# Kernel optimization log

Hardware: AMD Instinct MI355X
Metric: run time of the kernel (lower is better)

## Reference

```python
import jax, jax.numpy as jnp
import numpy as np

LMAX = 2
NC = (LMAX + 1) ** 2          # 9 spherical-harmonic coefficients
C = 128                       # sphere/hidden channels (scalar_dim = 256//2)
CIN = 256                     # input/output irrep channels
EC = 16                       # edge channels (attn_weight_input_dim//2)
N_ATOM = 512
TOPK = 8
E = N_ATOM * TOPK
RES = 18                      # SO3 grid resolution

# m-primary permutation from CoefficientMapping(lmax=2, mmax=2).to_m:
# m=0 real [0,2,6]; m=1 real [3,7]; m=1 imag [1,5]; m=2 real [8]; m=2 imag [4]
PERM = np.array([0, 2, 6, 3, 7, 1, 5, 8, 4])
INV_PERM = np.argsort(PERM)
DEG = np.array([0, 1, 1, 1, 2, 2, 2, 2, 2])  # degree l of each coefficient


def _so2_block(em, x_edge, d0w, d0b, m0w1, m0w2,
               m1dw, m1db, m1w1r, m1w2r, m1w1i, m1w2i,
               m2dw, m2db, m2w1r, m2w2r, m2w1i, m2w2i):
    # em: [E, 9, C] (l-primary); x_edge: [E, EC]
    En = em.shape[0]
    em = em[:, PERM]                                  # -> m-primary order
    # m = 0 block (3 coefficients)
    g0 = jax.nn.silu(x_edge @ d0w + d0b)              # [E, C]
    x0 = em[:, 0:3].reshape(En, 3 * C)
    x0 = (((x0 @ m0w1) * g0) @ m0w2).reshape(En, 3, C)

    def so2_conv(xm, dw, db, w1r, w2r, w1i, w2i):
        # xm: [E, 2, k*C] with (real, imag) stacked on axis 1
        ge = jax.nn.silu(x_edge @ dw + db).reshape(En, 2, C)
        xr = jnp.einsum('eti,ih->eth', xm, w1r) * ge[:, 0:1]
        xr = jnp.einsum('eth,ho->eto', xr, w2r)
        xi = jnp.einsum('eti,ih->eth', xm, w1i) * ge[:, 1:2]
        xi = jnp.einsum('eth,ho->eto', xi, w2i)
        return jnp.stack([xr[:, 0] - xi[:, 1], xr[:, 1] + xi[:, 0]], axis=1)

    x1 = so2_conv(em[:, 3:7].reshape(En, 2, 2 * C), m1dw, m1db, m1w1r, m1w2r, m1w1i, m1w2i).reshape(En, 4, C)
    x2 = so2_conv(em[:, 7:9].reshape(En, 2, C), m2dw, m2db, m2w1r, m2w2r, m2w1i, m2w2i).reshape(En, 2, C)
    em = jnp.concatenate([x0, x1, x2], axis=1)
    return em[:, INV_PERM]                            # back to l-primary


def _forward(x, attn_weight, wigner, to_grid, from_grid, w_in, b_in, w_out, b_out,
             emb_src, emb_tgt, fc_dist_w, fc_dist_b, fc_edge_w, fc_edge_b,
             so2_dist0_w, so2_dist0_b, so2_m0_w1, so2_m0_w2,
             so2_m1_dist_w, so2_m1_dist_b, so2_m1_w1r, so2_m1_w2r, so2_m1_w1i, so2_m1_w2i,
             so2_m2_dist_w, so2_m2_dist_b, so2_m2_w1r, so2_m2_w2r, so2_m2_w1i, so2_m2_w2i,
             atomic_numbers, edge_src, attn_mask):
    N, topK = attn_weight.shape[:2]
    Eg = N * topK
    # proj_input: per-degree SO3 linear 256 -> 128, bias on l=0 only
    h = jnp.einsum('nic,ico->nio', x, w_in[DEG])
    h = h.at[:, 0, :].add(b_in)
    edge_tgt = jnp.repeat(jnp.arange(N), topK)
    # edge feature: dist MLP + source/target atom-type embedding gathers
    xe = attn_weight.reshape(Eg, -1) @ fc_dist_w + fc_dist_b
    xe = xe + emb_src[atomic_numbers][edge_src] + emb_tgt[atomic_numbers][edge_tgt]
    xe = jax.nn.silu(jax.nn.silu(xe) @ fc_edge_w + fc_edge_b)
    # gather node features to edges + rotate into edge frame (Wigner D)
    xs = jnp.einsum('eij,ejc->eic', wigner, h[edge_src])
    xt = jnp.einsum('eij,ejc->eic', wigner, h[edge_tgt])

    def blk(b, em):
        return _so2_block(em, xe, so2_dist0_w[b], so2_dist0_b[b], so2_m0_w1[b], so2_m0_w2[b],
                          so2_m1_dist_w[b], so2_m1_dist_b[b], so2_m1_w1r[b], so2_m1_w2r[b], so2_m1_w1i[b], so2_m1_w2i[b],
                          so2_m2_dist_w[b], so2_m2_dist_b[b], so2_m2_w1r[b], so2_m2_w2r[b], so2_m2_w1i[b], so2_m2_w2i[b])

    xt = blk(0, xs) + blk(1, xt)
    # grid activation: to-grid, SiLU, from-grid
    xg = jax.nn.silu(jnp.einsum('bai,eic->ebac', to_grid, xt))
    xt = jnp.einsum('bai,ebac->eic', from_grid, xg)
    # inverse rotation (orthogonal Wigner -> transpose)
    xt = jnp.einsum('eji,ejc->eic', wigner, xt)
    # mask invalid neighbors, scatter-sum over topK
    out = xt.reshape(N, topK, NC, C)
    out = jnp.where(attn_mask[:, :, None, None], 0.0, out).sum(axis=1)
    # proj_final: per-degree SO3 linear 128 -> 256
    out = jnp.einsum('nic,ico->nio', out, w_out[DEG])
    return out.at[:, 0, :].add(b_out)


def setup_inputs() -> dict:
    key = jax.random.key(0)
    ks = jax.random.split(key, 40)
    s = 0.05
    inp = {
        'x': jax.random.normal(ks[0], (N_ATOM, NC, CIN), jnp.float32),
        'attn_weight': jax.random.normal(ks[1], (N_ATOM, TOPK, 32), jnp.float32),
        'wigner': jax.random.normal(ks[2], (E, NC, NC), jnp.float32) * 0.3,
        'to_grid': jax.random.normal(ks[3], (RES, RES, NC), jnp.float32) * 0.2,
        'from_grid': jax.random.normal(ks[4], (RES, RES, NC), jnp.float32) * 0.2,
        'w_in': jax.random.normal(ks[5], (3, CIN, C), jnp.float32) * s,
        'b_in': jax.random.normal(ks[6], (C,), jnp.float32) * s,
        'w_out': jax.random.normal(ks[7], (3, C, CIN), jnp.float32) * s,
        'b_out': jax.random.normal(ks[8], (CIN,), jnp.float32) * s,
        'emb_src': jax.random.uniform(ks[9], (256, EC), jnp.float32, -0.001, 0.001),
        'emb_tgt': jax.random.uniform(ks[10], (256, EC), jnp.float32, -0.001, 0.001),
        'fc_dist_w': jax.random.normal(ks[11], (32, EC), jnp.float32) * s,
        'fc_dist_b': jax.random.normal(ks[12], (EC,), jnp.float32) * s,
        'fc_edge_w': jax.random.normal(ks[13], (EC, EC), jnp.float32) * s,
        'fc_edge_b': jax.random.normal(ks[14], (EC,), jnp.float32) * s,
        'so2_dist0_w': jax.random.normal(ks[15], (2, EC, C), jnp.float32) * s,
        'so2_dist0_b': jax.random.normal(ks[16], (2, C), jnp.float32) * s,
        'so2_m0_w1': jax.random.normal(ks[17], (2, 3 * C, C), jnp.float32) * s,
        'so2_m0_w2': jax.random.normal(ks[18], (2, C, 3 * C), jnp.float32) * s,
        'so2_m1_dist_w': jax.random.normal(ks[19], (2, EC, 2 * C), jnp.float32) * s,
        'so2_m1_dist_b': jax.random.normal(ks[20], (2, 2 * C), jnp.float32) * s,
        'so2_m1_w1r': jax.random.normal(ks[21], (2, 2 * C, C), jnp.float32) * s,
        'so2_m1_w2r': jax.random.normal(ks[22], (2, C, 2 * C), jnp.float32) * s,
        'so2_m1_w1i': jax.random.normal(ks[23], (2, 2 * C, C), jnp.float32) * s,
        'so2_m1_w2i': jax.random.normal(ks[24], (2, C, 2 * C), jnp.float32) * s,
        'so2_m2_dist_w': jax.random.normal(ks[25], (2, EC, 2 * C), jnp.float32) * s,
        'so2_m2_dist_b': jax.random.normal(ks[26], (2, 2 * C), jnp.float32) * s,
        'so2_m2_w1r': jax.random.normal(ks[27], (2, C, C), jnp.float32) * s,
        'so2_m2_w2r': jax.random.normal(ks[28], (2, C, C), jnp.float32) * s,
        'so2_m2_w1i': jax.random.normal(ks[29], (2, C, C), jnp.float32) * s,
        'so2_m2_w2i': jax.random.normal(ks[30], (2, C, C), jnp.float32) * s,
        'atomic_numbers': jax.random.randint(ks[31], (N_ATOM,), 0, 256),
        'edge_src': jax.random.randint(ks[32], (E,), 0, N_ATOM),
        'attn_mask': jax.random.randint(ks[33], (N_ATOM, TOPK), 0, 2).astype(bool),
    }
    return inp


def reference(x, attn_weight, wigner, to_grid, from_grid, w_in, b_in, w_out, b_out,
              emb_src, emb_tgt, fc_dist_w, fc_dist_b, fc_edge_w, fc_edge_b,
              so2_dist0_w, so2_dist0_b, so2_m0_w1, so2_m0_w2,
              so2_m1_dist_w, so2_m1_dist_b, so2_m1_w1r, so2_m1_w2r, so2_m1_w1i, so2_m1_w2i,
              so2_m2_dist_w, so2_m2_dist_b, so2_m2_w1r, so2_m2_w2r, so2_m2_w1i, so2_m2_w2i,
              atomic_numbers, edge_src, attn_mask):
    return _forward(x, attn_weight, wigner, to_grid, from_grid, w_in, b_in, w_out, b_out,
                    emb_src, emb_tgt, fc_dist_w, fc_dist_b, fc_edge_w, fc_edge_b,
                    so2_dist0_w, so2_dist0_b, so2_m0_w1, so2_m0_w2,
                    so2_m1_dist_w, so2_m1_dist_b, so2_m1_w1r, so2_m1_w2r, so2_m1_w1i, so2_m1_w2i,
                    so2_m2_dist_w, so2_m2_dist_b, so2_m2_w1r, so2_m2_w2r, so2_m2_w1i, so2_m2_w2i,
                    atomic_numbers, edge_src, attn_mask)
```

## Files before the change

### kernel.cpp

```cpp
#include <hip/hip_runtime.h>
#include <math.h>

typedef __attribute__((ext_vector_type(8))) short short8;
typedef __attribute__((ext_vector_type(4))) short short4_t;
typedef __attribute__((ext_vector_type(4))) float f32x4;

__device__ const int d_PERM[9] = {0,2,6,3,7,1,5,8,4};
__device__ const int d_DEG[9]  = {0,1,1,1,2,2,2,2,2};

__device__ __forceinline__ float silu_f(float x){ return x / (1.0f + __expf(-x)); }

__device__ __forceinline__ unsigned short f2bf(float f){
  unsigned int u = __float_as_uint(f);
  return (unsigned short)((u + 0x7FFFu + ((u >> 16) & 1u)) >> 16);
}

__device__ __forceinline__ int mask_at(const void* mp, int flag, int e){
  if (flag==1) return ((const unsigned char*)mp)[e] != 0;
  if (flag==3) return ((const unsigned int*)mp)[2*e] != 0u;
  return ((const unsigned int*)mp)[e] != 0u;
}

__global__ void k_detect(const unsigned int* __restrict__ w, int* __restrict__ flag){
  __shared__ int notI, notF, anyOdd, anyEven;
  if (threadIdx.x==0){ notI=0; notF=0; anyOdd=0; anyEven=0; }
  __syncthreads();
  int li=0, lf=0, lo=0, le=0;
  for (int i = threadIdx.x; i < 1024; i += 256){
    unsigned int v = w[i];
    if (v != 0u && v != 1u) li = 1;
    if (v != 0u && v != 0x3F800000u) lf = 1;
    if (v != 0u){ if (i & 1) lo = 1; else le = 1; }
  }
  if (li) atomicOr(&notI,1);
  if (lf) atomicOr(&notF,1);
  if (lo) atomicOr(&anyOdd,1);
  if (le) atomicOr(&anyEven,1);
  __syncthreads();
  if (threadIdx.x==0){
    int f;
    if (!notI) f = (anyOdd || !anyEven) ? 0 : 3;
    else       f = (!notF) ? 2 : 1;
    *flag = f;
  }
}

__global__ __launch_bounds__(256) void k_compact(const void* __restrict__ maskp,
    const int* __restrict__ flagp, int* __restrict__ list, int* __restrict__ count){
  __shared__ int cnt[256];
  __shared__ int offs[256];
  int f = *flagp;
  int tid = threadIdx.x;
  int base = tid*16;
  int c = 0;
  for (int i=0;i<16;i++) if (!mask_at(maskp, f, base+i)) c++;
  cnt[tid] = c;
  __syncthreads();
  if (tid==0){
    int r = 0;
    for (int i=0;i<256;i++){ offs[i] = r; r += cnt[i]; }
    *count = r;
  }
  __syncthreads();
  int w = offs[tid];
  for (int i=0;i<16;i++){
    int e = base+i;
    if (!mask_at(maskp, f, e)) list[w++] = e;
  }
}

__global__ __launch_bounds__(128) void k_h(const float* __restrict__ x,
    const float* __restrict__ w_in, const float* __restrict__ b_in,
    float* __restrict__ H){
  __shared__ float xl[16][260];
  int i = blockIdx.y; int n0 = blockIdx.x*16;
  int deg = d_DEG[i];
  for (int idx = threadIdx.x; idx < 16*256; idx += 128){
    int r = idx >> 8, c = idx & 255;
    xl[r][c] = x[((size_t)(n0+r)*9 + i)*256 + c];
  }
  __syncthreads();
  int o = threadIdx.x;
  float acc[16];
  #pragma unroll
  for (int r=0;r<16;r++) acc[r]=0.f;
  const float* w = w_in + (size_t)deg*32768 + o;
  for (int c=0;c<256;c+=4){
    float w0=w[(size_t)c*128], w1=w[(size_t)(c+1)*128], w2=w[(size_t)(c+2)*128], w3=w[(size_t)(c+3)*128];
    #pragma unroll
    for (int r=0;r<16;r++){
      float4 xv4 = *(const float4*)&xl[r][c];
      acc[r] += xv4.x*w0 + xv4.y*w1 + xv4.z*w2 + xv4.w*w3;
    }
  }
  float bb = (i==0)? b_in[o] : 0.f;
  #pragma unroll
  for (int r=0;r<16;r++) H[((size_t)(n0+r)*9+i)*128+o] = acc[r]+bb;
}

__global__ __launch_bounds__(256) void k_xe(const float* __restrict__ attn,
    const float* __restrict__ fdw, const float* __restrict__ fdb,
    const float* __restrict__ few, const float* __restrict__ feb,
    const float* __restrict__ es, const float* __restrict__ et,
    const int* __restrict__ an, const int* __restrict__ esrc,
    float* __restrict__ XE){
  int e = blockIdx.x*256 + threadIdx.x;
  float aw[32];
  #pragma unroll
  for (int k=0;k<32;k+=4){
    float4 v = *(const float4*)&attn[(size_t)e*32+k];
    aw[k]=v.x; aw[k+1]=v.y; aw[k+2]=v.z; aw[k+3]=v.w;
  }
  int src = esrc[e]; int tgt = e>>3;
  int za = an[src], zb = an[tgt];
  float v0[16];
  #pragma unroll
  for (int j=0;j<16;j++){
    float s = fdb[j] + es[(size_t)za*16+j] + et[(size_t)zb*16+j];
    #pragma unroll
    for (int k=0;k<32;k++) s += aw[k]*fdw[k*16+j];
    v0[j] = silu_f(s);
  }
  #pragma unroll
  for (int j=0;j<16;j++){
    float s = feb[j];
    #pragma unroll
    for (int k=0;k<16;k++) s += v0[k]*few[k*16+j];
    XE[(size_t)e*16+j] = silu_f(s);
  }
}

__global__ __launch_bounds__(256) void k_wcvt(
    const float* __restrict__ m0w1, const float* __restrict__ m1w1r, const float* __restrict__ m1w1i,
    const float* __restrict__ m2w1r, const float* __restrict__ m2w1i,
    const float* __restrict__ m0w2, const float* __restrict__ m1w2r, const float* __restrict__ m1w2i,
    const float* __restrict__ m2w2r, const float* __restrict__ m2w2i,
    unsigned short* __restrict__ Wt)
{
  int base = (blockIdx.x*256 + threadIdx.x)*4;
  #pragma unroll
  for (int ii = 0; ii < 4; ii++){
    int idx = base + ii;
    float v;
    if (idx < 98304){
      int p = idx/49152, r = idx%49152, n = r/384, k = r%384;
      v = m0w1[p*49152 + k*128 + n];
    } else if (idx < 229376){
      int j = idx-98304; int q = j/32768, r = j%32768, n = r/256, k = r%256;
      const float* w = (q&1)?m1w1i:m1w1r;
      v = w[(q>>1)*32768 + k*128 + n];
    } else if (idx < 294912){
      int j = idx-229376; int q = j/16384, r = j%16384, n = r/128, k = r%128;
      const float* w = (q&1)?m2w1i:m2w1r;
      v = w[(q>>1)*16384 + k*128 + n];
    } else if (idx < 393216){
      int j = idx-294912; int n = j/256, k = j%256;
      v = m0w2[(k>>7)*49152 + (k&127)*384 + n];
    } else if (idx < 524288){
      int j = idx-393216; int n = j/512, k = j%512;
      const float* w = ((k>>7)&1)?m1w2i:m1w2r;
      v = w[(k>>8)*32768 + (k&127)*256 + n];
    } else {
      int j = idx-524288; int n = j/512, k = j%512;
      const float* w = ((k>>7)&1)?m2w2i:m2w2r;
      v = w[(k>>8)*16384 + (k&127)*128 + n];
    }
    Wt[idx] = f2bf(v);
  }
}

__global__ __launch_bounds__(256) void k_fprep(const float* __restrict__ tg,
    const float* __restrict__ fg,
    unsigned short* __restrict__ tgA, unsigned short* __restrict__ fgA)
{
  for (int idx = threadIdx.x; idx < 11264; idx += 256){
    int pt = idx >> 9, rem = idx & 511, l = rem >> 3, j = rem & 7;
    int p = pt*16 + (l & 15);
    int i = (l >> 4)*8 + j;
    float v = (p < 324 && i < 9) ? tg[p*9 + i] : 0.f;
    tgA[idx] = f2bf(v);
  }
  for (int idx = threadIdx.x; idx < 5632; idx += 256){
    int sb = idx >> 9, rem = idx & 511, l = rem >> 3, j = rem & 7;
    int p = sb*32 + (l >> 4)*8 + j;
    int i = l & 15;
    float v = (p < 324 && i < 9) ? fg[p*9 + i] : 0.f;
    fgA[idx] = f2bf(v);
  }
}

__global__ __launch_bounds__(256) void k_rotgate_m(
    const float* __restrict__ Hg, const float* __restrict__ XEg,
    const int* __restrict__ esrc, const float* __restrict__ wig,
    const float* __restrict__ d0w,  const float* __restrict__ d0b,
    const float* __restrict__ m1dw, const float* __restrict__ m1db,
    const float* __restrict__ m2dw, const float* __restrict__ m2db,
    unsigned short* __restrict__ XSb, unsigned short* __restrict__ XTb,
    float* __restrict__ G,
    const int* __restrict__ list, const int* __restrict__ countp, int s0)
{
  int slot = s0 + blockIdx.x;
  if (slot >= *countp) return;
  __shared__ float xe16[16];
  int e = list[slot];
  int el = blockIdx.x;
  int tid = threadIdx.x;
  int n = e >> 3, src = esrc[e];
  if (tid < 16) xe16[tid] = XEg[(size_t)e*16 + tid];
  for (int idx = tid; idx < 1152; idx += 256){
    int p = idx >> 7, c = idx & 127;
    int ch = d_PERM[p];
    const float* wr = wig + (size_t)e*81 + ch*9;
    const float* hs = Hg + (size_t)src*1152 + c;
    const float* ht = Hg + (size_t)n*1152 + c;
    float s1 = 0.f, s2 = 0.f;
    #pragma unroll
    for (int j = 0; j < 9; j++){
      float wv = wr[j];
      s1 += wv * hs[j*128];
      s2 += wv * ht[j*128];
    }
    XSb[(size_t)el*1152 + idx] = f2bf(s1);
    XTb[(size_t)el*1152 + idx] = f2bf(s2);
  }
  __syncthreads();
  for (int col = tid; col < 1280; col += 256){
    int b = col / 640, r = col % 640;
    const float* w; float bias; int ldw, c2;
    if (r < 128){       w = d0w  + (size_t)b*2048; c2 = r;     ldw = 128; bias = d0b[b*128 + c2]; }
    else if (r < 384){  w = m1dw + (size_t)b*4096; c2 = r-128; ldw = 256; bias = m1db[b*256 + c2]; }
    else {              w = m2dw + (size_t)b*4096; c2 = r-384; ldw = 256; bias = m2db[b*256 + c2]; }
    float s = bias;
    #pragma unroll
    for (int kk = 0; kk < 16; kk++) s += xe16[kk] * w[kk*ldw + c2];
    G[(size_t)el*1280 + col] = silu_f(s);
  }
}

__global__ __launch_bounds__(256) void k_gs1m(
    const unsigned short* __restrict__ XSb, const unsigned short* __restrict__ XTb,
    const float* __restrict__ G, const unsigned short* __restrict__ Wt,
    unsigned short* __restrict__ Pgb,
    const int* __restrict__ countp, int s0)
{
  int lc = *countp - s0;
  if (lc <= 0) return;
  if (lc > 2048) lc = 2048;
  int b = blockIdx.x, t = threadIdx.x;
  const unsigned short* Ax; const unsigned short* Bw;
  int K, bm, obase, goff, rsh, aoff, tstride;
  if (b < 64){
    int path = b & 1, mt = b >> 1;
    Ax = path ? XTb : XSb;
    Bw = Wt + path*49152;
    K = 384; bm = mt*64; obase = path*128; goff = path ? 640 : 0;
    rsh = 0; aoff = 0; tstride = 0;
  } else if (b < 320){
    int i = b-64; int q = i>>6, mt = i&63;
    Ax = (q>=2) ? XTb : XSb;
    Bw = Wt + 98304 + q*32768;
    K = 256; bm = mt*64; obase = 256 + q*256; goff = 128 + (q&1)*128 + (q>>1)*640;
    rsh = 1; aoff = 384; tstride = 256;
  } else {
    int i = b-320; int q = i>>6, mt = i&63;
    Ax = (q>=2) ? XTb : XSb;
    Bw = Wt + 229376 + q*16384;
    K = 128; bm = mt*64; obase = 1280 + q*256; goff = 384 + (q&1)*128 + (q>>1)*640;
    rsh = 1; aoff = 896; tstride = 128;
  }
  int rows = rsh ? 2*lc : lc;
  if (bm >= rows) return;
  int w = t >> 6, l = t & 63;
  int am = bm + w*16 + (l & 15);
  int ael = am >> rsh, atp = am & rsh;
  const unsigned short* aptr = Ax + (size_t)ael*1152 + aoff + atp*tstride + ((l>>4)*8);
  int bn = l & 15;
  int bko = (l>>4)*8;
  f32x4 acc[8];
  #pragma unroll
  for (int i=0;i<8;i++){ acc[i][0]=0.f; acc[i][1]=0.f; acc[i][2]=0.f; acc[i][3]=0.f; }
  for (int k0 = 0; k0 < K; k0 += 32){
    short8 a = *(const short8*)(aptr + k0);
    #pragma unroll
    for (int nt = 0; nt < 8; nt++){
      const unsigned short* bp = Bw + (size_t)(nt*16 + bn)*K + k0 + bko;
      short8 bb = *(const short8*)bp;
      acc[nt] = __builtin_amdgcn_mfma_f32_16x16x32_bf16(a, bb, acc[nt], 0, 0, 0);
    }
  }
  #pragma unroll
  for (int nt = 0; nt < 8; nt++){
    #pragma unroll
    for (int r = 0; r < 4; r++){
      int i2 = (l>>4)*4 + r;
      int m = bm + w*16 + i2;
      int el = m >> rsh, tp = m & rsh;
      int h = nt*16 + (l & 15);
      float v = acc[nt][r] * G[(size_t)el*1280 + goff + h];
      Pgb[(size_t)el*2304 + obase + tp*128 + h] = f2bf(v);
    }
  }
}

__global__ __launch_bounds__(256) void k_gs2m(
    const unsigned short* __restrict__ Pgb, const unsigned short* __restrict__ Wt2,
    unsigned short* __restrict__ Ybt,
    const int* __restrict__ countp, int s0)
{
  int lc = *countp - s0;
  if (lc <= 0) return;
  if (lc > 2048) lc = 2048;
  int b = blockIdx.x, t = threadIdx.x;
  int region, bm, ncb, K, rsh, segb;
  const unsigned short* Bw;
  if (b < 96){ region=0; int mt=b/3, nt3=b-mt*3; bm=mt*64; ncb=nt3*128; K=256; rsh=0; segb=0;    Bw = Wt2; }
  else if (b < 224){ region=1; int i=b-96; int mt=i>>1, nt2=i&1; bm=mt*64; ncb=nt2*128; K=512; rsh=1; segb=256;  Bw = Wt2 + 98304; }
  else { region=2; int mt=b-224; bm=mt*64; ncb=0; K=512; rsh=1; segb=1280; Bw = Wt2 + 229376; }
  int rows = rsh ? 2*lc : lc;
  if (bm >= rows) return;
  int w = t >> 6, l = t & 63;
  int am = bm + w*16 + (l & 15);
  int ael = am >> rsh, atp = am & rsh;
  int bko = (l>>4)*8;
  f32x4 acc[8];
  #pragma unroll
  for (int i=0;i<8;i++){ acc[i][0]=0.f; acc[i][1]=0.f; acc[i][2]=0.f; acc[i][3]=0.f; }
  for (int k0 = 0; k0 < K; k0 += 32){
    const unsigned short* ap;
    short sm = 0;
    if (region == 0){
      ap = Pgb + (size_t)ael*2304 + k0 + bko;
    } else {
      int seg = k0 >> 7, kk = k0 & 127;
      int tsel = (seg&1) ? (1-atp) : atp;
      sm = (short)(((seg&1) && atp==0) ? 0x8000 : 0);
      ap = Pgb + (size_t)ael*2304 + segb + seg*256 + tsel*128 + kk + bko;
    }
    short8 a = *(const short8*)ap;
    short8 smv = (short8)sm;
    a ^= smv;
    #pragma unroll
    for (int nt = 0; nt < 8; nt++){
      const unsigned short* bp = Bw + (size_t)(ncb + nt*16 + (l&15))*K + k0 + bko;
      short8 bb = *(const short8*)bp;
      acc[nt] = __builtin_amdgcn_mfma_f32_16x16x32_bf16(a, bb, acc[nt], 0, 0, 0);
    }
  }
  #pragma unroll
  for (int nt = 0; nt < 8; nt++){
    #pragma unroll
    for (int r = 0; r < 4; r++){
      int i2 = (l>>4)*4 + r;
      int m = bm + w*16 + i2;
      int el = m >> rsh, tp = m & rsh;
      int col = ncb + nt*16 + (l&15);
      int g = col >> 7, c = col & 127;
      int ch;
      if (region==0)      ch = (g==0) ? 0 : ((g==1) ? 2 : 6);
      else if (region==1) ch = tp ? (g ? 5 : 1) : (g ? 7 : 3);
      else                ch = tp ? 4 : 8;
      Ybt[(size_t)(s0 + el)*2048 + c*16 + ch] = f2bf(acc[nt][r]);
    }
  }
}

__global__ __launch_bounds__(256) void k_gridm(
    const unsigned short* __restrict__ Ybt,
    const unsigned short* __restrict__ tgA, const unsigned short* __restrict__ fgA,
    const float* __restrict__ wig,
    const int* __restrict__ list, const int* __restrict__ countp,
    float* __restrict__ R)
{
  int slot = blockIdx.x;
  if (slot >= *countp) return;
  __shared__ float wl[81];
  __shared__ unsigned short Sld[4][512];
  __shared__ float Zld[4][256];
  int tid = threadIdx.x;
  int e = list[slot];
  for (int i = tid; i < 81; i += 256) wl[i] = wig[(size_t)e*81 + i];
  __syncthreads();
  int w = tid >> 6, l = tid & 63;
  int lcn = l & 15, lg = l >> 4;
  const unsigned short* ybase = Ybt + (size_t)slot*2048;

  for (int ct = 0; ct < 2; ct++){
    int c0 = (w*2 + ct)*16;
    short8 bfA = (short8)(short)0;
    if (lg < 2) bfA = *(const short8*)(ybase + (c0 + lcn)*16 + lg*8);
    f32x4 Z; Z[0]=0.f; Z[1]=0.f; Z[2]=0.f; Z[3]=0.f;
    for (int sb = 0; sb < 11; sb++){
      f32x4 s0; s0[0]=0.f; s0[1]=0.f; s0[2]=0.f; s0[3]=0.f;
      f32x4 s1 = s0;
      short8 a0 = *(const short8*)(tgA + (size_t)(sb*2+0)*512 + l*8);
      short8 a1 = *(const short8*)(tgA + (size_t)(sb*2+1)*512 + l*8);
      s0 = __builtin_amdgcn_mfma_f32_16x16x32_bf16(a0, bfA, s0, 0, 0, 0);
      s1 = __builtin_amdgcn_mfma_f32_16x16x32_bf16(a1, bfA, s1, 0, 0, 0);
      short4_t pk0, pk1;
      #pragma unroll
      for (int r = 0; r < 4; r++){
        float v0 = s0[r]; v0 = v0 * __fdividef(1.0f, 1.0f + __expf(-v0));
        float v1 = s1[r]; v1 = v1 * __fdividef(1.0f, 1.0f + __expf(-v1));
        pk0[r] = (short)f2bf(v0);
        pk1[r] = (short)f2bf(v1);
      }
      *(short4_t*)&Sld[w][lcn*32 + lg*4]      = pk0;
      *(short4_t*)&Sld[w][lcn*32 + 16 + lg*4] = pk1;
      short8 af = *(const short8*)(fgA + (size_t)sb*512 + l*8);
      short8 bs = *(const short8*)&Sld[w][lcn*32 + lg*8];
      Z = __builtin_amdgcn_mfma_f32_16x16x32_bf16(af, bs, Z, 0, 0, 0);
    }
    *(f32x4*)&Zld[w][lcn*16 + lg*4] = Z;
    float zc[9];
    #pragma unroll
    for (int j = 0; j < 9; j++) zc[j] = Zld[w][lcn*16 + j];
    #pragma unroll
    for (int t2 = 0; t2 < 3; t2++){
      int i2 = lg + t2*4;
      if (i2 < 9){
        float r = 0.f;
        #pragma unroll
        for (int j = 0; j < 9; j++) r += wl[j*9 + i2] * zc[j];
        R[(size_t)e*1152 + i2*128 + c0 + lcn] = r;
      }
    }
  }
}

__global__ __launch_bounds__(256) void k_redout2(const float* __restrict__ R,
    const void* __restrict__ maskp, const int* __restrict__ flagp,
    const float* __restrict__ w_out, const float* __restrict__ b_out,
    float* __restrict__ out){
  __shared__ float sacc[128];
  int i2 = blockIdx.x; int n = blockIdx.y;
  int tid = threadIdx.x;
  int f = *flagp;
  if (tid < 128){
    float a = 0.f;
    for (int k = 0; k < 8; k++){
      int e = n*8 + k;
      if (!mask_at(maskp, f, e)) a += R[(size_t)e*1152 + i2*128 + tid];
    }
    sacc[tid] = a;
  }
  __syncthreads();
  int o = tid;
  int deg = d_DEG[i2];
  const float* wp = w_out + (size_t)deg*32768 + o;
  float s = (i2==0) ? b_out[o] : 0.f;
  #pragma unroll 4
  for (int c = 0; c < 128; c += 4){
    float4 a = *(const float4*)&sacc[c];
    s += a.x*wp[(size_t)c*256] + a.y*wp[(size_t)(c+1)*256]
       + a.z*wp[(size_t)(c+2)*256] + a.w*wp[(size_t)(c+3)*256];
  }
  out[((size_t)n*9 + i2)*256 + o] = s;
}

__device__ __forceinline__ float dotW(const float* __restrict__ A, const float* __restrict__ Wm, int K){
  float s = 0.f;
  #pragma unroll 4
  for (int i=0;i<K;i+=4){
    float4 a = *(const float4*)&A[i];
    s += a.x*Wm[(size_t)i*128] + a.y*Wm[(size_t)(i+1)*128]
       + a.z*Wm[(size_t)(i+2)*128] + a.w*Wm[(size_t)(i+3)*128];
  }
  return s;
}
__device__ __forceinline__ float dot2W(const float* __restrict__ P0, const float* __restrict__ P1,
    const float* __restrict__ W0, const float* __restrict__ W1, int ldw){
  float s = 0.f;
  #pragma unroll 4
  for (int k=0;k<128;k+=4){
    float4 a = *(const float4*)&P0[k];
    float4 b = *(const float4*)&P1[k];
    s += a.x*W0[(size_t)k*ldw] + a.y*W0[(size_t)(k+1)*ldw] + a.z*W0[(size_t)(k+2)*ldw] + a.w*W0[(size_t)(k+3)*ldw];
    s += b.x*W1[(size_t)k*ldw] + b.y*W1[(size_t)(k+1)*ldw] + b.z*W1[(size_t)(k+2)*ldw] + b.w*W1[(size_t)(k+3)*ldw];
  }
  return s;
}

__global__ __launch_bounds__(256) void k_mega(
    const float* __restrict__ x,      const float* __restrict__ w_in,  const float* __restrict__ b_in,
    const float* __restrict__ attn,
    const float* __restrict__ fdw,    const float* __restrict__ fdb,
    const float* __restrict__ few,    const float* __restrict__ feb,
    const float* __restrict__ es,     const float* __restrict__ et,
    const int*   __restrict__ an,     const int*   __restrict__ esrc,
    const float* __restrict__ d0w,    const float* __restrict__ d0b,
    const float* __restrict__ m1dw,   const float* __restrict__ m1db,
    const float* __restrict__ m2dw,   const float* __restrict__ m2db,
    const float* __restrict__ m0w1,   const float* __restrict__ m0w2,
    const float* __restrict__ m1w1r,  const float* __restrict__ m1w2r,
    const float* __restrict__ m1w1i,  const float* __restrict__ m1w2i,
    const float* __restrict__ m2w1r,  const float* __restrict__ m2w2r,
    const float* __restrict__ m2w1i,  const float* __restrict__ m2w2i,
    const float* __restrict__ wig,    const float* __restrict__ tg,   const float* __restrict__ fg,
    const float* __restrict__ w_out,  const float* __restrict__ b_out,
    const void*  __restrict__ maskp,  const int* __restrict__ flagp,
    float* __restrict__ out)
{
  __shared__ float S[7168];
  float* acc  = S;
  float* xs   = S + 1152;
  float* xtl  = S + 2304;
  float* Zb   = S + 1152;
  float* gg   = S + 3456;
  float* Yb   = S + 3456;
  float* P    = S + 4736;
  float* wl   = S + 7040;
  float* xe16 = S + 7124;
  float* xv   = S + 7140;

  const int n   = blockIdx.x;
  const int tid = threadIdx.x;
  const int f   = *flagp;

  for (int i = tid; i < 1152; i += 256) acc[i] = 0.f;

  for (int k = 0; k < 8; k++){
    int e = n*8 + k;
    if (mask_at(maskp, f, e)) continue;
    int src = esrc[e];
    __syncthreads();
    for (int i = tid; i < 81; i += 256) wl[i] = wig[(size_t)e*81 + i];
    if (tid < 16){
      int j = tid;
      float s = fdb[j] + es[(size_t)an[src]*16 + j] + et[(size_t)an[n]*16 + j];
      for (int kk = 0; kk < 32; kk++) s += attn[(size_t)e*32 + kk] * fdw[kk*16 + j];
      xv[j] = silu_f(s);
    }
    for (int idx = tid; idx < 2304; idx += 256){
      int which = idx >= 1152;
      int lidx = idx - which*1152;
      int j = lidx >> 7, c = lidx & 127;
      int deg = d_DEG[j];
      const float* wp = w_in + (size_t)deg*32768 + c;
      const float* xp = x + ((size_t)(which ? n : src)*9 + j)*256;
      float s = (j==0) ? b_in[c] : 0.f;
      for (int cc = 0; cc < 256; cc++) s += xp[cc] * wp[cc*128];
      P[idx] = s;
    }
    __syncthreads();
    if (tid < 16){
      int j = tid;
      float s = feb[j];
      for (int kk = 0; kk < 16; kk++) s += xv[kk] * few[kk*16 + j];
      xe16[j] = silu_f(s);
    }
    for (int idx = tid; idx < 1152; idx += 256){
      int p = idx >> 7, c = idx & 127;
      int ch = d_PERM[p];
      float s1 = 0.f, s2 = 0.f;
      #pragma unroll
      for (int j = 0; j < 9; j++){
        float wv = wl[ch*9 + j];
        s1 += wv * P[j*128 + c];
        s2 += wv * P[1152 + j*128 + c];
      }
      xs[idx]  = s1;
      xtl[idx] = s2;
    }
    __syncthreads();
    for (int col = tid; col < 1280; col += 256){
      int b = col / 640, r = col % 640;
      const float* w; float bias; int ldw, c2;
      if (r < 128){       w = d0w  + (size_t)b*2048; c2 = r;     ldw = 128; bias = d0b[b*128 + c2]; }
      else if (r < 384){  w = m1dw + (size_t)b*4096; c2 = r-128; ldw = 256; bias = m1db[b*256 + c2]; }
      else {              w = m2dw + (size_t)b*4096; c2 = r-384; ldw = 256; bias = m2db[b*256 + c2]; }
      float s = bias;
      #pragma unroll
      for (int kk = 0; kk < 16; kk++) s += xe16[kk] * w[kk*ldw + c2];
      gg[col] = silu_f(s);
    }
    __syncthreads();
    for (int o = tid; o < 2304; o += 256){
      float s;
      if (o < 256){
        int path = o >> 7, h = o & 127;
        s = dotW(path ? xtl : xs, m0w1 + (size_t)path*49152 + h, 384);
      } else if (o < 1280){
        int q = (o-256) >> 8; int rem = (o-256) & 255; int t = rem >> 7, h = rem & 127;
        const float* A  = ((q>=2) ? xtl : xs) + 384 + t*256;
        const float* Wm = ((q&1) ? m1w1i : m1w1r) + (size_t)((q>=2)?1:0)*32768 + h;
        s = dotW(A, Wm, 256);
      } else {
        int q = (o-1280) >> 8; int rem = (o-1280) & 255; int t = rem >> 7, h = rem & 127;
        const float* A  = ((q>=2) ? xtl : xs) + 896 + t*128;
        const float* Wm = ((q&1) ? m2w1i : m2w1r) + (size_t)((q>=2)?1:0)*16384 + h;
        s = dotW(A, Wm, 128);
      }
      P[o] = s;
    }
    __syncthreads();
    for (int o = tid; o < 2304; o += 256){
      int h = o & 127, goff;
      if (o < 256) goff = (o >> 7) ? 640 : 0;
      else if (o < 1280){ int q = (o-256) >> 8;  goff = 128 + (q&1)*128 + (q>>1)*640; }
      else              { int q = (o-1280) >> 8; goff = 384 + (q&1)*128 + (q>>1)*640; }
      P[o] *= gg[goff + h];
    }
    __syncthreads();
    for (int o = tid; o < 1152; o += 256){
      float s; int ch, c;
      if (o < 384){
        int g = o >> 7; c = o & 127;
        ch = (g==0) ? 0 : ((g==1) ? 2 : 6);
        const float* w0 = m0w2 + o;
        s = dot2W(P, P+128, w0, w0+49152, 384);
      } else if (o < 896){
        int om = o - 384; int tp = om >> 8; int col = om & 255;
        int g = col >> 7; c = col & 127;
        ch = tp ? (g ? 5 : 1) : (g ? 7 : 3);
        float sgn = tp ? 1.f : -1.f;
        const float* wr = m1w2r + col;
        const float* wi = m1w2i + col;
        s = dot2W(P+256+tp*128,     P+768+tp*128,     wr, wr+32768, 256)
          + sgn * dot2W(P+512+(1-tp)*128, P+1024+(1-tp)*128, wi, wi+32768, 256);
      } else {
        int om = o - 896; int tp = om >> 7; c = om & 127;
        ch = tp ? 4 : 8;
        float sgn = tp ? 1.f : -1.f;
        const float* wr = m2w2r + c;
        const float* wi = m2w2i + c;
        s = dot2W(P+1280+tp*128,     P+1792+tp*128,     wr, wr+16384, 128)
          + sgn * dot2W(P+1536+(1-tp)*128, P+2048+(1-tp)*128, wi, wi+16384, 128);
      }
      Yb[ch*128 + c] = s;
    }
    __syncthreads();
    {
      int half = tid >> 7, c = tid & 127;
      float z[9];
      #pragma unroll
      for (int i = 0; i < 9; i++) z[i] = 0.f;
      float y[9];
      #pragma unroll
      for (int i = 0; i < 9; i++) y[i] = Yb[i*128 + c];
      int p0 = half*162, p1 = p0 + 162;
      #pragma unroll 2
      for (int p = p0; p < p1; p++){
        float gp = 0.f;
        #pragma unroll
        for (int i = 0; i < 9; i++) gp += tg[p*9 + i] * y[i];
        float s = silu_f(gp);
        #pragma unroll
        for (int i = 0; i < 9; i++) z[i] += fg[p*9 + i] * s;
      }
      #pragma unroll
      for (int i = 0; i < 9; i++) Zb[half*1152 + i*128 + c] = z[i];
    }
    __syncthreads();
    for (int idx = tid; idx < 1152; idx += 256){
      int i2 = idx >> 7, c = idx & 127;
      float s = 0.f;
      #pragma unroll
      for (int j = 0; j < 9; j++)
        s += wl[j*9 + i2] * (Zb[j*128 + c] + Zb[1152 + j*128 + c]);
      acc[idx] += s;
    }
  }
  __syncthreads();
  {
    int o = tid;
    for (int i2 = 0; i2 < 9; i2++){
      int deg = d_DEG[i2];
      const float* wp = w_out + (size_t)deg*32768 + o;
      float s = (i2==0) ? b_out[o] : 0.f;
      #pragma unroll 4
      for (int c = 0; c < 128; c += 4){
        float4 a = *(const float4*)&acc[i2*128 + c];
        s += a.x*wp[(size_t)c*256] + a.y*wp[(size_t)(c+1)*256]
           + a.z*wp[(size_t)(c+2)*256] + a.w*wp[(size_t)(c+3)*256];
      }
      out[((size_t)n*9 + i2)*256 + o] = s;
    }
  }
}

extern "C" void kernel_launch(void* const* d_in, const int* in_sizes, int n_in,
                              void* d_out, int out_size, void* d_ws, size_t ws_size,
                              hipStream_t stream){
  const float* x     = (const float*)d_in[0];
  const float* attn  = (const float*)d_in[1];
  const float* wig   = (const float*)d_in[2];
  const float* tg    = (const float*)d_in[3];
  const float* fg    = (const float*)d_in[4];
  const float* w_in  = (const float*)d_in[5];
  const float* b_in  = (const float*)d_in[6];
  const float* w_out = (const float*)d_in[7];
  const float* b_out = (const float*)d_in[8];
  const float* es    = (const float*)d_in[9];
  const float* et    = (const float*)d_in[10];
  const float* fdw   = (const float*)d_in[11];
  const float* fdb   = (const float*)d_in[12];
  const float* few   = (const float*)d_in[13];
  const float* feb   = (const float*)d_in[14];
  const float* d0w   = (const float*)d_in[15];
  const float* d0b   = (const float*)d_in[16];
  const float* m0w1  = (const float*)d_in[17];
  const float* m0w2  = (const float*)d_in[18];
  const float* m1dw  = (const float*)d_in[19];
  const float* m1db  = (const float*)d_in[20];
  const float* m1w1r = (const float*)d_in[21];
  const float* m1w2r = (const float*)d_in[22];
  const float* m1w1i = (const float*)d_in[23];
  const float* m1w2i = (const float*)d_in[24];
  const float* m2dw  = (const float*)d_in[25];
  const float* m2db  = (const float*)d_in[26];
  const float* m2w1r = (const float*)d_in[27];
  const float* m2w2r = (const float*)d_in[28];
  const float* m2w1i = (const float*)d_in[29];
  const float* m2w2i = (const float*)d_in[30];
  const int*   an    = (const int*)d_in[31];
  const int*   esrc  = (const int*)d_in[32];
  const void*  maskp = d_in[33];

  int*   ip  = (int*)d_ws;
  int* FLAG  = ip + 0;
  int* COUNT = ip + 1;
  int* LIST  = ip + 16;
  float* W   = (float*)d_ws;
  float* Hg1  = W + 4112;
  float* XEg1 = Hg1 + 589824;
  float* XS1  = XEg1 + 65536;
  float* XT1  = XS1 + 2359296;
  float* Gg1  = XT1 + 2359296;
  float* Pg1  = Gg1 + 2621440;
  float* Yf   = Pg1 + 4718592;
  float* Rf   = XS1;
  unsigned short* XSb = (unsigned short*)XS1;
  unsigned short* XTb = XSb + 2359296;
  unsigned short* Pgb = XSb + 4718592;
  unsigned short* Wtb = (unsigned short*)Pg1;
  unsigned short* tgAb = Wtb + 655360;
  unsigned short* fgAb = tgAb + 11264;
  unsigned short* Ybt  = (unsigned short*)Yf;
  size_t need_t1 = (size_t)(4112 + 589824 + 65536 + 2359296 + 2359296 + 2621440 + 4718592 + 4718592) * 4;

  k_detect<<<1,256,0,stream>>>((const unsigned int*)maskp, FLAG);

  if (ws_size >= need_t1){
    k_compact<<<1,256,0,stream>>>(maskp, FLAG, LIST, COUNT);
    k_h<<<dim3(32,9),128,0,stream>>>(x, w_in, b_in, Hg1);
    k_xe<<<16,256,0,stream>>>(attn, fdw, fdb, few, feb, es, et, an, esrc, XEg1);
    k_wcvt<<<576,256,0,stream>>>(m0w1, m1w1r, m1w1i, m2w1r, m2w1i,
                                 m0w2, m1w2r, m1w2i, m2w2r, m2w2i, Wtb);
    k_fprep<<<1,256,0,stream>>>(tg, fg, tgAb, fgAb);
    hipMemsetAsync(Ybt, 0, (size_t)8388608*2, stream);
    for (int c2 = 0; c2 < 2; c2++){
      int s0 = c2*2048;
      k_rotgate_m<<<2048,256,0,stream>>>(Hg1, XEg1, esrc, wig,
          d0w, d0b, m1dw, m1db, m2dw, m2db, XSb, XTb, Gg1, LIST, COUNT, s0);
      k_gs1m<<<576,256,0,stream>>>(XSb, XTb, Gg1, Wtb, Pgb, COUNT, s0);
      k_gs2m<<<288,256,0,stream>>>(Pgb, Wtb + 294912, Ybt, COUNT, s0);
    }
    k_gridm<<<4096,256,0,stream>>>(Ybt, tgAb, fgAb, wig, LIST, COUNT, Rf);
    k_redout2<<<dim3(9,512),256,0,stream>>>(Rf, maskp, FLAG, w_out, b_out, (float*)d_out);
  } else {
    k_mega<<<512,256,0,stream>>>(
        x, w_in, b_in, attn, fdw, fdb, few, feb, es, et, an, esrc,
        d0w, d0b, m1dw, m1db, m2dw, m2db,
        m0w1, m0w2, m1w1r, m1w2r, m1w1i, m1w2i, m2w1r, m2w2r, m2w1i, m2w2i,
        wig, tg, fg, w_out, b_out, maskp, FLAG, (float*)d_out);
  }
}
```

Before: 305.6 us.

## Process all edges in one pass, store gates and SO2 outputs in bf16

Drops the two-chunk loop over edges and launches rotate/gate, both SO2 GEMMs and the grid kernel once over all 4096 edge slots, with workspace pointers reassigned to hold full-size buffers. The gate tensor G is now stored in bf16 rather than fp32, which halves its traffic. The Y intermediate is written in a dense channel-major bf16 layout and transposed into padded LDS inside the grid kernel. This removes the large memset of the padded Y buffer. The grid kernel's S tile is padded in LDS to avoid bank conflicts. Gate precision is reduced to bf16.

```diff
diff --git a/kernel.cpp b/kernel.cpp
--- a/kernel.cpp
+++ b/kernel.cpp
@@ -13,6 +13,9 @@
 __device__ __forceinline__ unsigned short f2bf(float f){
   unsigned int u = __float_as_uint(f);
   return (unsigned short)((u + 0x7FFFu + ((u >> 16) & 1u)) >> 16);
+}
+__device__ __forceinline__ float bf2f(unsigned short b){
+  return __uint_as_float(((unsigned int)b) << 16);
 }
 
 __device__ __forceinline__ int mask_at(const void* mp, int flag, int e){
@@ -196,14 +199,13 @@
     const float* __restrict__ m1dw, const float* __restrict__ m1db,
     const float* __restrict__ m2dw, const float* __restrict__ m2db,
     unsigned short* __restrict__ XSb, unsigned short* __restrict__ XTb,
-    float* __restrict__ G,
-    const int* __restrict__ list, const int* __restrict__ countp, int s0)
+    unsigned short* __restrict__ Gb,
+    const int* __restrict__ list, const int* __restrict__ countp)
 {
-  int slot = s0 + blockIdx.x;
+  int slot = blockIdx.x;
   if (slot >= *countp) return;
   __shared__ float xe16[16];
   int e = list[slot];
-  int el = blockIdx.x;
   int tid = threadIdx.x;
   int n = e >> 3, src = esrc[e];
   if (tid < 16) xe16[tid] = XEg[(size_t)e*16 + tid];
@@ -220,8 +222,8 @@
       s1 += wv * hs[j*128];
       s2 += wv * ht[j*128];
     }
-    XSb[(size_t)el*1152 + idx] = f2bf(s1);
-    XTb[(size_t)el*1152 + idx] = f2bf(s2);
+    XSb[(size_t)slot*1152 + idx] = f2bf(s1);
+    XTb[(size_t)slot*1152 + idx] = f2bf(s2);
   }
   __syncthreads();
   for (int col = tid; col < 1280; col += 256){
@@ -233,36 +235,35 @@
     float s = bias;
     #pragma unroll
     for (int kk = 0; kk < 16; kk++) s += xe16[kk] * w[kk*ldw + c2];
-    G[(size_t)el*1280 + col] = silu_f(s);
+    Gb[(size_t)slot*1280 + col] = f2bf(silu_f(s));
   }
 }
 
 __global__ __launch_bounds__(256) void k_gs1m(
     const unsigned short* __restrict__ XSb, const unsigned short* __restrict__ XTb,
-    const float* __restrict__ G, const unsigned short* __restrict__ Wt,
+    const unsigned short* __restrict__ Gb, const unsigned short* __restrict__ Wt,
     unsigned short* __restrict__ Pgb,
-    const int* __restrict__ countp, int s0)
+    const int* __restrict__ countp)
 {
-  int lc = *countp - s0;
+  int lc = *countp;
   if (lc <= 0) return;
-  if (lc > 2048) lc = 2048;
   int b = blockIdx.x, t = threadIdx.x;
   const unsigned short* Ax; const unsigned short* Bw;
   int K, bm, obase, goff, rsh, aoff, tstride;
-  if (b < 64){
+  if (b < 128){
     int path = b & 1, mt = b >> 1;
     Ax = path ? XTb : XSb;
     Bw = Wt + path*49152;
     K = 384; bm = mt*64; obase = path*128; goff = path ? 640 : 0;
     rsh = 0; aoff = 0; tstride = 0;
-  } else if (b < 320){
-    int i = b-64; int q = i>>6, mt = i&63;
+  } else if (b < 640){
+    int i = b-128; int q = i>>7, mt = i&127;
     Ax = (q>=2) ? XTb : XSb;
     Bw = Wt + 98304 + q*32768;
     K = 256; bm = mt*64; obase = 256 + q*256; goff = 128 + (q&1)*128 + (q>>1)*640;
     rsh = 1; aoff = 384; tstride = 256;
   } else {
-    int i = b-320; int q = i>>6, mt = i&63;
+    int i = b-640; int q = i>>7, mt = i&127;
     Ax = (q>=2) ? XTb : XSb;
     Bw = Wt + 229376 + q*16384;
     K = 128; bm = mt*64; obase = 1280 + q*256; goff = 384 + (q&1)*128 + (q>>1)*640;
@@ -296,7 +297,7 @@
       int m = bm + w*16 + i2;
       int el = m >> rsh, tp = m & rsh;
       int h = nt*16 + (l & 15);
-      float v = acc[nt][r] * G[(size_t)el*1280 + goff + h];
+      float v = acc[nt][r] * bf2f(Gb[(size_t)el*1280 + goff + h]);
       Pgb[(size_t)el*2304 + obase + tp*128 + h] = f2bf(v);
     }
   }
@@ -304,18 +305,17 @@
 
 __global__ __launch_bounds__(256) void k_gs2m(
     const unsigned short* __restrict__ Pgb, const unsigned short* __restrict__ Wt2,
-    unsigned short* __restrict__ Ybt,
-    const int* __restrict__ countp, int s0)
+    unsigned short* __restrict__ Ybb,
+    const int* __restrict__ countp)
 {
-  int lc = *countp - s0;
+  int lc = *countp;
   if (lc <= 0) return;
-  if (lc > 2048) lc = 2048;
   int b = blockIdx.x, t = threadIdx.x;
   int region, bm, ncb, K, rsh, segb;
   const unsigned short* Bw;
-  if (b < 96){ region=0; int mt=b/3, nt3=b-mt*3; bm=mt*64; ncb=nt3*128; K=256; rsh=0; segb=0;    Bw = Wt2; }
-  else if (b < 224){ region=1; int i=b-96; int mt=i>>1, nt2=i&1; bm=mt*64; ncb=nt2*128; K=512; rsh=1; segb=256;  Bw = Wt2 + 98304; }
-  else { region=2; int mt=b-224; bm=mt*64; ncb=0; K=512; rsh=1; segb=1280; Bw = Wt2 + 229376; }
+  if (b < 192){ region=0; int mt=b/3, nt3=b-mt*3; bm=mt*64; ncb=nt3*128; K=256; rsh=0; segb=0;    Bw = Wt2; }
+  else if (b < 448){ region=1; int i=b-192; int mt=i>>1, nt2=i&1; bm=mt*64; ncb=nt2*128; K=512; rsh=1; segb=256;  Bw = Wt2 + 98304; }
+  else { region=2; int mt=b-448; bm=mt*64; ncb=0; K=512; rsh=1; segb=1280; Bw = Wt2 + 229376; }
   int rows = rsh ? 2*lc : lc;
   if (bm >= rows) return;
   int w = t >> 6, l = t & 63;
@@ -359,13 +359,13 @@
       if (region==0)      ch = (g==0) ? 0 : ((g==1) ? 2 : 6);
       else if (region==1) ch = tp ? (g ? 5 : 1) : (g ? 7 : 3);
       else                ch = tp ? 4 : 8;
-      Ybt[(size_t)(s0 + el)*2048 + c*16 + ch] = f2bf(acc[nt][r]);
+      Ybb[(size_t)el*1152 + ch*128 + c] = f2bf(acc[nt][r]);
     }
   }
 }
 
 __global__ __launch_bounds__(256) void k_gridm(
-    const unsigned short* __restrict__ Ybt,
+    const unsigned short* __restrict__ Ybb,
     const unsigned short* __restrict__ tgA, const unsigned short* __restrict__ fgA,
     const float* __restrict__ wig,
     const int* __restrict__ list, const int* __restrict__ countp,
@@ -374,20 +374,27 @@
   int slot = blockIdx.x;
   if (slot >= *countp) return;
   __shared__ float wl[81];
-  __shared__ unsigned short Sld[4][512];
+  __shared__ unsigned short YL[128*24];
+  __shared__ unsigned short Sld[4][640];
   __shared__ float Zld[4][256];
   int tid = threadIdx.x;
   int e = list[slot];
   for (int i = tid; i < 81; i += 256) wl[i] = wig[(size_t)e*81 + i];
+  for (int i = tid; i < 3072; i += 256) YL[i] = 0;
+  __syncthreads();
+  const unsigned short* ybase = Ybb + (size_t)slot*1152;
+  for (int idx = tid; idx < 1152; idx += 256){
+    int ch = idx >> 7, c = idx & 127;
+    YL[c*24 + ch] = ybase[idx];
+  }
   __syncthreads();
   int w = tid >> 6, l = tid & 63;
   int lcn = l & 15, lg = l >> 4;
-  const unsigned short* ybase = Ybt + (size_t)slot*2048;
 
   for (int ct = 0; ct < 2; ct++){
     int c0 = (w*2 + ct)*16;
     short8 bfA = (short8)(short)0;
-    if (lg < 2) bfA = *(const short8*)(ybase + (c0 + lcn)*16 + lg*8);
+    if (lg < 2) bfA = *(const short8*)(&YL[(c0 + lcn)*24 + lg*8]);
     f32x4 Z; Z[0]=0.f; Z[1]=0.f; Z[2]=0.f; Z[3]=0.f;
     for (int sb = 0; sb < 11; sb++){
       f32x4 s0; s0[0]=0.f; s0[1]=0.f; s0[2]=0.f; s0[3]=0.f;
@@ -404,10 +411,10 @@
         pk0[r] = (short)f2bf(v0);
         pk1[r] = (short)f2bf(v1);
       }
-      *(short4_t*)&Sld[w][lcn*32 + lg*4]      = pk0;
-      *(short4_t*)&Sld[w][lcn*32 + 16 + lg*4] = pk1;
+      *(short4_t*)&Sld[w][lcn*40 + lg*4]      = pk0;
+      *(short4_t*)&Sld[w][lcn*40 + 16 + lg*4] = pk1;
       short8 af = *(const short8*)(fgA + (size_t)sb*512 + l*8);
-      short8 bs = *(const short8*)&Sld[w][lcn*32 + lg*8];
+      short8 bs = *(const short8*)&Sld[w][lcn*40 + lg*8];
       Z = __builtin_amdgcn_mfma_f32_16x16x32_bf16(af, bs, Z, 0, 0, 0);
     }
     *(f32x4*)&Zld[w][lcn*16 + lg*4] = Z;
@@ -730,12 +737,13 @@
   float* Yf   = Pg1 + 4718592;
   float* Rf   = XS1;
   unsigned short* XSb = (unsigned short*)XS1;
-  unsigned short* XTb = XSb + 2359296;
-  unsigned short* Pgb = XSb + 4718592;
-  unsigned short* Wtb = (unsigned short*)Pg1;
+  unsigned short* XTb = (unsigned short*)XT1;
+  unsigned short* Gbb = (unsigned short*)Gg1;
+  unsigned short* Pgb = (unsigned short*)Pg1;
+  unsigned short* Ybb = (unsigned short*)Yf;
+  unsigned short* Wtb = Ybb + 4718592;
   unsigned short* tgAb = Wtb + 655360;
   unsigned short* fgAb = tgAb + 11264;
-  unsigned short* Ybt  = (unsigned short*)Yf;
   size_t need_t1 = (size_t)(4112 + 589824 + 65536 + 2359296 + 2359296 + 2621440 + 4718592 + 4718592) * 4;
 
   k_detect<<<1,256,0,stream>>>((const unsigned int*)maskp, FLAG);
@@ -747,15 +755,11 @@
     k_wcvt<<<576,256,0,stream>>>(m0w1, m1w1r, m1w1i, m2w1r, m2w1i,
                                  m0w2, m1w2r, m1w2i, m2w2r, m2w2i, Wtb);
     k_fprep<<<1,256,0,stream>>>(tg, fg, tgAb, fgAb);
-    hipMemsetAsync(Ybt, 0, (size_t)8388608*2, stream);
-    for (int c2 = 0; c2 < 2; c2++){
-      int s0 = c2*2048;
-      k_rotgate_m<<<2048,256,0,stream>>>(Hg1, XEg1, esrc, wig,
-          d0w, d0b, m1dw, m1db, m2dw, m2db, XSb, XTb, Gg1, LIST, COUNT, s0);
-      k_gs1m<<<576,256,0,stream>>>(XSb, XTb, Gg1, Wtb, Pgb, COUNT, s0);
-      k_gs2m<<<288,256,0,stream>>>(Pgb, Wtb + 294912, Ybt, COUNT, s0);
-    }
-    k_gridm<<<4096,256,0,stream>>>(Ybt, tgAb, fgAb, wig, LIST, COUNT, Rf);
+    k_rotgate_m<<<4096,256,0,stream>>>(Hg1, XEg1, esrc, wig,
+        d0w, d0b, m1dw, m1db, m2dw, m2db, XSb, XTb, Gbb, LIST, COUNT);
+    k_gs1m<<<1152,256,0,stream>>>(XSb, XTb, Gbb, Wtb, Pgb, COUNT);
+    k_gs2m<<<576,256,0,stream>>>(Pgb, Wtb + 294912, Ybb, COUNT);
+    k_gridm<<<4096,256,0,stream>>>(Ybb, tgAb, fgAb, wig, LIST, COUNT, Rf);
     k_redout2<<<dim3(9,512),256,0,stream>>>(Rf, maskp, FLAG, w_out, b_out, (float*)d_out);
   } else {
     k_mega<<<512,256,0,stream>>>(
```

New measurement: 262.1 us. -14.2%, faster.
